# Performance work log

Measured on AMD Instinct MI355X. Metric: run time of the kernel, lower is better.

The kernel has to match this reference:

```python
import jax, jax.numpy as jnp
import numpy as np

DIM = 3072
NUM_HEADS = 24
HEAD_DIM = DIM // NUM_HEADS  # 128
SEQ = 2048
BATCH = 1


def rms_norm(x, scale):
    # compute in fp32 like the torch module
    xf = x.astype(jnp.float32)
    rrms = jax.lax.rsqrt(jnp.mean(xf * xf, axis=-1, keepdims=True) + 1e-6)
    return (xf * rrms).astype(x.dtype) * scale


def apply_rope(xq, xk, pe):
    # xq, xk: [B, H, L, D]; pe: [B, 1, L, D//2, 2, 2]
    shp = xq.shape
    xq_ = xq.reshape(*shp[:-1], -1, 1, 2).astype(jnp.float32)
    xk_ = xk.reshape(*shp[:-1], -1, 1, 2).astype(jnp.float32)
    xq_out = pe[..., 0] * xq_[..., 0] + pe[..., 1] * xq_[..., 1]
    xk_out = pe[..., 0] * xk_[..., 0] + pe[..., 1] * xk_[..., 1]
    return xq_out.reshape(shp).astype(xq.dtype), xk_out.reshape(shp).astype(xk.dtype)


def setup_inputs() -> dict:
    key = jax.random.key(0)
    ks = jax.random.split(key, 6)
    s = 1.0 / np.sqrt(DIM)
    return {
        "x": jax.random.normal(ks[0], (BATCH, SEQ, DIM), dtype=jnp.float32),
        "pe": jax.random.normal(ks[1], (BATCH, 1, SEQ, HEAD_DIM // 2, 2, 2), dtype=jnp.float32),
        "w_qkv": jax.random.normal(ks[2], (3 * DIM, DIM), dtype=jnp.float32) * s,
        "w_proj": jax.random.normal(ks[3], (DIM, DIM), dtype=jnp.float32) * s,
        "b_proj": jax.random.normal(ks[4], (DIM,), dtype=jnp.float32) * 0.01,
        "q_scale": jnp.ones((HEAD_DIM,), dtype=jnp.float32),
        "k_scale": jnp.ones((HEAD_DIM,), dtype=jnp.float32),
    }


def reference(x, pe, w_qkv, w_proj, b_proj, q_scale, k_scale):
    B, L, _ = x.shape
    # fused qkv projection (qkv_bias=False)
    qkv = jnp.einsum("bld,ed->ble", x, w_qkv)  # [B, L, 3*DIM]
    qkv = qkv.reshape(B, L, 3, NUM_HEADS, HEAD_DIM)
    qkv = jnp.transpose(qkv, (2, 0, 3, 1, 4))  # [3, B, H, L, D]
    q, k, v = qkv[0], qkv[1], qkv[2]
    # QKNorm (RMSNorm on head_dim)
    q = rms_norm(q, q_scale).astype(v.dtype)
    k = rms_norm(k, k_scale).astype(v.dtype)
    # rope
    q, k = apply_rope(q, k, pe)
    # scaled dot-product attention
    scale = 1.0 / np.sqrt(HEAD_DIM)
    scores = jnp.einsum("bhqd,bhkd->bhqk", q, k) * scale
    probs = jax.nn.softmax(scores, axis=-1)
    out = jnp.einsum("bhqk,bhkd->bhqd", probs, v)
    out = jnp.transpose(out, (0, 2, 1, 3)).reshape(B, L, DIM)  # merge heads
    # output projection
    return jnp.einsum("bld,ed->ble", out, w_proj) + b_proj
```

## Files before the change

### kernel.cpp

```cpp
#include <hip/hip_runtime.h>

typedef __bf16 bf16;
typedef __attribute__((ext_vector_type(8))) __bf16 bf16x8;
typedef __attribute__((ext_vector_type(4))) float f32x4;

typedef __attribute__((address_space(1))) void gvoid_t;
typedef __attribute__((address_space(3))) void lvoid_t;

#define LDS_LOAD16(gp, lp) \
    __builtin_amdgcn_global_load_lds((gvoid_t*)(gp), (lvoid_t*)(lp), 16, 0, 0)

__global__ __launch_bounds__(256)
void f32_to_bf16(const float* __restrict__ in, bf16* __restrict__ out, int n8)
{
    const int i = blockIdx.x * 256 + threadIdx.x;
    if (i >= n8) return;
    const float4 a = ((const float4*)in)[i * 2];
    const float4 b = ((const float4*)in)[i * 2 + 1];
    bf16x8 o;
    o[0] = (bf16)a.x; o[1] = (bf16)a.y; o[2] = (bf16)a.z; o[3] = (bf16)a.w;
    o[4] = (bf16)b.x; o[5] = (bf16)b.y; o[6] = (bf16)b.z; o[7] = (bf16)b.w;
    *(bf16x8*)(out + (size_t)i * 8) = o;
}

template <int BIAS, typename CT>
__global__ __launch_bounds__(256, 2)
void gemm_bt(const bf16* __restrict__ A, const bf16* __restrict__ B,
             const float* __restrict__ bias, CT* __restrict__ C,
             int K, int ldc)
{
    __shared__ bf16 sA[128 * 32];
    __shared__ bf16 sB[128 * 32];
    const int tid  = threadIdx.x;
    const int lane = tid & 63;
    const int wid  = tid >> 6;
    const int m0 = blockIdx.y * 128;
    const int n0 = blockIdx.x * 128;
    const int wm = (wid >> 1) * 64;
    const int wn = (wid & 1) * 64;
    const int l15   = lane & 15;
    const int quad8 = (lane >> 4) * 8;

    f32x4 acc[4][4] = {};

    for (int k0 = 0; k0 < K; k0 += 32) {
#pragma unroll
        for (int t = 0; t < 2; ++t) {
            const int e  = (t * 4 + wid) * 512;
            const int ge = e + lane * 8;
            const int r = ge >> 5, c = ge & 31;
            LDS_LOAD16(A + (size_t)(m0 + r) * K + k0 + c, sA + e);
            LDS_LOAD16(B + (size_t)(n0 + r) * K + k0 + c, sB + e);
        }
        __syncthreads();

        bf16x8 af[4], bfr[4];
#pragma unroll
        for (int i = 0; i < 4; ++i) {
            af[i]  = *(const bf16x8*)(sA + (wm + i * 16 + l15) * 32 + quad8);
            bfr[i] = *(const bf16x8*)(sB + (wn + i * 16 + l15) * 32 + quad8);
        }
#pragma unroll
        for (int i = 0; i < 4; ++i)
#pragma unroll
            for (int j = 0; j < 4; ++j)
                acc[i][j] = __builtin_amdgcn_mfma_f32_16x16x32_bf16(af[i], bfr[j], acc[i][j], 0, 0, 0);
        __syncthreads();
    }

    const int rowBase = m0 + wm + (lane >> 4) * 4;
    const int colBase = n0 + wn + l15;
#pragma unroll
    for (int j = 0; j < 4; ++j) {
        const int col = colBase + j * 16;
        const float bv = BIAS ? bias[col] : 0.0f;
#pragma unroll
        for (int i = 0; i < 4; ++i) {
            const int row = rowBase + i * 16;
#pragma unroll
            for (int r = 0; r < 4; ++r)
                C[(size_t)(row + r) * ldc + col] = (CT)(acc[i][j][r] + bv);
        }
    }
}

template <int BIAS, typename CT>
__global__ __launch_bounds__(512, 4)
void gemm128_bt(const bf16* __restrict__ A, const bf16* __restrict__ B,
                const float* __restrict__ bias, CT* __restrict__ C,
                int K, int ldc)
{
    __shared__ bf16 sA[2 * 128 * 64];
    __shared__ bf16 sB[2 * 192 * 64];

    const int tid  = threadIdx.x;
    const int lane = tid & 63;
    const int wid  = tid >> 6;
    const int m0 = blockIdx.y * 128;
    const int n0 = blockIdx.x * 192;
    const int wm = (wid >> 2) * 64;
    const int wn = (wid & 3) * 48;
    const int l15  = lane & 15;
    const int quad = lane >> 4;

    int aoff[2], boff[3];
    int adst[2], bdst[3];
#pragma unroll
    for (int t = 0; t < 2; ++t) {
        const int slot = t * 512 + tid;
        const int r  = slot >> 3;
        const int cg = (slot & 7) ^ (r & 7);
        aoff[t] = (m0 + r) * K + cg * 8;
        adst[t] = (t * 512 + wid * 64) * 8;
    }
#pragma unroll
    for (int t = 0; t < 3; ++t) {
        const int slot = t * 512 + tid;
        const int r  = slot >> 3;
        const int cg = (slot & 7) ^ (r & 7);
        boff[t] = (n0 + r) * K + cg * 8;
        bdst[t] = (t * 512 + wid * 64) * 8;
    }

#define STA(t, kt, buf) LDS_LOAD16(A + (size_t)aoff[t] + (kt) * 64, sA + (buf) * 8192  + adst[t])
#define STB(t, kt, buf) LDS_LOAD16(B + (size_t)boff[t] + (kt) * 64, sB + (buf) * 12288 + bdst[t])

    int aRd[2], bRd[2];
#pragma unroll
    for (int kk = 0; kk < 2; ++kk) {
        const int pcg = (kk * 4 + quad) ^ (l15 & 7);
        aRd[kk] = (wm + l15) * 128 + pcg * 16;
        bRd[kk] = (wn + l15) * 128 + pcg * 16;
    }

    f32x4 acc[4][3] = {};

#pragma unroll
    for (int t = 0; t < 2; ++t) STA(t, 0, 0);
#pragma unroll
    for (int t = 0; t < 3; ++t) STB(t, 0, 0);
    asm volatile("s_waitcnt vmcnt(0)" ::: "memory");

    const int NT = K >> 6;
#pragma unroll 1
    for (int u = 0; u < NT; ++u) {
        const int b = u & 1;
        __builtin_amdgcn_s_barrier();
        if (u + 1 < NT) {
            STA(0, u + 1, b ^ 1); STA(1, u + 1, b ^ 1);
            STB(0, u + 1, b ^ 1); STB(1, u + 1, b ^ 1); STB(2, u + 1, b ^ 1);
        }
        __builtin_amdgcn_sched_barrier(0);

        bf16x8 af[4][2], bfr[3][2];
#pragma unroll
        for (int mi = 0; mi < 2; ++mi)
#pragma unroll
            for (int kk = 0; kk < 2; ++kk)
                af[mi][kk] = *(const bf16x8*)((const char*)sA + b * 16384 +
                                              aRd[kk] + mi * 2048);
#pragma unroll
        for (int nf = 0; nf < 3; ++nf)
#pragma unroll
            for (int kk = 0; kk < 2; ++kk)
                bfr[nf][kk] = *(const bf16x8*)((const char*)sB + b * 24576 +
                                               bRd[kk] + nf * 2048);
        __builtin_amdgcn_sched_barrier(0);
#pragma unroll
        for (int mi = 2; mi < 4; ++mi)
#pragma unroll
            for (int kk = 0; kk < 2; ++kk)
                af[mi][kk] = *(const bf16x8*)((const char*)sA + b * 16384 +
                                              aRd[kk] + mi * 2048);
        __builtin_amdgcn_sched_barrier(0);

        asm volatile("s_waitcnt lgkmcnt(4)" ::: "memory");
        __builtin_amdgcn_sched_barrier(0);
        __builtin_amdgcn_s_setprio(1);
#pragma unroll
        for (int mi = 0; mi < 2; ++mi)
#pragma unroll
            for (int nf = 0; nf < 3; ++nf)
#pragma unroll
                for (int kk = 0; kk < 2; ++kk)
                    acc[mi][nf] = __builtin_amdgcn_mfma_f32_16x16x32_bf16(
                        af[mi][kk], bfr[nf][kk], acc[mi][nf], 0, 0, 0);
        __builtin_amdgcn_sched_barrier(0);
        asm volatile("s_waitcnt lgkmcnt(0)" ::: "memory");
        __builtin_amdgcn_sched_barrier(0);
#pragma unroll
        for (int mi = 2; mi < 4; ++mi)
#pragma unroll
            for (int nf = 0; nf < 3; ++nf)
#pragma unroll
                for (int kk = 0; kk < 2; ++kk)
                    acc[mi][nf] = __builtin_amdgcn_mfma_f32_16x16x32_bf16(
                        af[mi][kk], bfr[nf][kk], acc[mi][nf], 0, 0, 0);
        __builtin_amdgcn_s_setprio(0);
        __builtin_amdgcn_sched_barrier(0);
        asm volatile("s_waitcnt vmcnt(0)" ::: "memory");
    }
#undef STA
#undef STB

    const int rowBase = m0 + wm + quad * 4;
    const int colBase = n0 + wn + l15;
#pragma unroll
    for (int nf = 0; nf < 3; ++nf) {
        const int col = colBase + nf * 16;
        const float bv = BIAS ? bias[col] : 0.0f;
#pragma unroll
        for (int mf = 0; mf < 4; ++mf) {
            const int row = rowBase + mf * 16;
#pragma unroll
            for (int r = 0; r < 4; ++r)
                C[(size_t)(row + r) * ldc + col] = (CT)(acc[mf][nf][r] + bv);
        }
    }
}

template <int BIAS, typename CT>
__global__ __launch_bounds__(512, 4)
void gemm64_bt(const bf16* __restrict__ A, const bf16* __restrict__ B,
               const float* __restrict__ bias, CT* __restrict__ C,
               int K, int ldc)
{
    __shared__ bf16 sA[2 * 64 * 64];
    __shared__ bf16 sB[2 * 192 * 64];

    const int tid  = threadIdx.x;
    const int lane = tid & 63;
    const int wid  = tid >> 6;
    const int m0 = blockIdx.y * 64;
    const int n0 = blockIdx.x * 192;
    const int wm = (wid >> 2) * 32;
    const int wn = (wid & 3) * 48;
    const int l15  = lane & 15;
    const int quad = lane >> 4;

    int aoff, adst;
    {
        const int slot = tid;
        const int r  = slot >> 3;
        const int cg = (slot & 7) ^ (r & 7);
        aoff = (m0 + r) * K + cg * 8;
        adst = (wid * 64) * 8;
    }
    int boff[3], bdst[3];
#pragma unroll
    for (int t = 0; t < 3; ++t) {
        const int slot = t * 512 + tid;
        const int r  = slot >> 3;
        const int cg = (slot & 7) ^ (r & 7);
        boff[t] = (n0 + r) * K + cg * 8;
        bdst[t] = (t * 512 + wid * 64) * 8;
    }

#define STA64(kt, buf)    LDS_LOAD16(A + (size_t)aoff    + (kt) * 64, sA + (buf) * 4096  + adst)
#define STB64(t, kt, buf) LDS_LOAD16(B + (size_t)boff[t] + (kt) * 64, sB + (buf) * 12288 + bdst[t])

    int aRd[2], bRd[2];
#pragma unroll
    for (int kk = 0; kk < 2; ++kk) {
        const int pcg = (kk * 4 + quad) ^ (l15 & 7);
        aRd[kk] = (wm + l15) * 128 + pcg * 16;
        bRd[kk] = (wn + l15) * 128 + pcg * 16;
    }

    f32x4 acc[2][3] = {};

    STA64(0, 0);
#pragma unroll
    for (int t = 0; t < 3; ++t) STB64(t, 0, 0);
    asm volatile("s_waitcnt vmcnt(0)" ::: "memory");

    const int NT = K >> 6;
#pragma unroll 1
    for (int u = 0; u < NT; ++u) {
        const int b = u & 1;
        __builtin_amdgcn_s_barrier();
        if (u + 1 < NT) {
            STA64(u + 1, b ^ 1);
            STB64(0, u + 1, b ^ 1); STB64(1, u + 1, b ^ 1); STB64(2, u + 1, b ^ 1);
        }
        __builtin_amdgcn_sched_barrier(0);

        bf16x8 af[2][2], bfr[3][2];
#pragma unroll
        for (int kk = 0; kk < 2; ++kk)
            af[0][kk] = *(const bf16x8*)((const char*)sA + b * 8192 + aRd[kk]);
#pragma unroll
        for (int nf = 0; nf < 3; ++nf)
#pragma unroll
            for (int kk = 0; kk < 2; ++kk)
                bfr[nf][kk] = *(const bf16x8*)((const char*)sB + b * 24576 +
                                               bRd[kk] + nf * 2048);
        __builtin_amdgcn_sched_barrier(0);
#pragma unroll
        for (int kk = 0; kk < 2; ++kk)
            af[1][kk] = *(const bf16x8*)((const char*)sA + b * 8192 + aRd[kk] + 2048);
        __builtin_amdgcn_sched_barrier(0);

        asm volatile("s_waitcnt lgkmcnt(2)" ::: "memory");
        __builtin_amdgcn_sched_barrier(0);
        __builtin_amdgcn_s_setprio(1);
#pragma unroll
        for (int nf = 0; nf < 3; ++nf)
#pragma unroll
            for (int kk = 0; kk < 2; ++kk)
                acc[0][nf] = __builtin_amdgcn_mfma_f32_16x16x32_bf16(
                    af[0][kk], bfr[nf][kk], acc[0][nf], 0, 0, 0);
        __builtin_amdgcn_sched_barrier(0);
        asm volatile("s_waitcnt lgkmcnt(0)" ::: "memory");
        __builtin_amdgcn_sched_barrier(0);
#pragma unroll
        for (int nf = 0; nf < 3; ++nf)
#pragma unroll
            for (int kk = 0; kk < 2; ++kk)
                acc[1][nf] = __builtin_amdgcn_mfma_f32_16x16x32_bf16(
                    af[1][kk], bfr[nf][kk], acc[1][nf], 0, 0, 0);
        __builtin_amdgcn_s_setprio(0);
        __builtin_amdgcn_sched_barrier(0);
        asm volatile("s_waitcnt vmcnt(0)" ::: "memory");
    }
#undef STA64
#undef STB64

    const int rowBase = m0 + wm + quad * 4;
    const int colBase = n0 + wn + l15;
#pragma unroll
    for (int nf = 0; nf < 3; ++nf) {
        const int col = colBase + nf * 16;
        const float bv = BIAS ? bias[col] : 0.0f;
#pragma unroll
        for (int mf = 0; mf < 2; ++mf) {
            const int row = rowBase + mf * 16;
#pragma unroll
            for (int r = 0; r < 4; ++r)
                C[(size_t)(row + r) * ldc + col] = (CT)(acc[mf][nf][r] + bv);
        }
    }
}

__global__ __launch_bounds__(256)
void qk_rope_rearrange(const bf16* __restrict__ qkv, const float* __restrict__ pe,
                       const float* __restrict__ qs, const float* __restrict__ ks,
                       bf16* __restrict__ Qh, bf16* __restrict__ Kh, bf16* __restrict__ Vt)
{
    const int lane = threadIdx.x & 63;
    const int wid  = threadIdx.x >> 6;
    const int idx  = blockIdx.x * 4 + wid;
    const int h = idx >> 11;
    const int l = idx & 2047;

    const size_t rowb = (size_t)l * 9216 + h * 128 + 2 * lane;
    const float q0 = (float)qkv[rowb];
    const float q1 = (float)qkv[rowb + 1];
    const float k0 = (float)qkv[rowb + 3072];
    const float k1 = (float)qkv[rowb + 3073];
    const bf16  v0 = qkv[rowb + 6144];
    const bf16  v1 = qkv[rowb + 6145];

    float ssq = q0 * q0 + q1 * q1;
    float ssk = k0 * k0 + k1 * k1;
#pragma unroll
    for (int off = 1; off < 64; off <<= 1) {
        ssq += __shfl_xor(ssq, off);
        ssk += __shfl_xor(ssk, off);
    }
    const float rq = rsqrtf(ssq * (1.0f / 128.0f) + 1e-6f);
    const float rk = rsqrtf(ssk * (1.0f / 128.0f) + 1e-6f);

    const float s0q = qs[2 * lane], s1q = qs[2 * lane + 1];
    const float s0k = ks[2 * lane], s1k = ks[2 * lane + 1];

    const float qn0 = (q0 * rq) * s0q;
    const float qn1 = (q1 * rq) * s1q;
    const float kn0 = (k0 * rk) * s0k;
    const float kn1 = (k1 * rk) * s1k;

    const float* pp = pe + ((size_t)l * 64 + lane) * 4;
    const float p00 = pp[0], p01 = pp[1];
    const float p10 = pp[2], p11 = pp[3];

    const bf16 qo0 = (bf16)(p00 * qn0 + p01 * qn1);
    const bf16 qo1 = (bf16)(p10 * qn0 + p11 * qn1);
    const bf16 ko0 = (bf16)(p00 * kn0 + p01 * kn1);
    const bf16 ko1 = (bf16)(p10 * kn0 + p11 * kn1);

    const size_t ob = ((size_t)h * 2048 + l) * 128 + 2 * lane;
    Qh[ob] = qo0; Qh[ob + 1] = qo1;
    Kh[ob] = ko0; Kh[ob + 1] = ko1;

    const size_t vb = ((size_t)h * 128 + 2 * lane) * 2048 + l;
    Vt[vb]        = v0;
    Vt[vb + 2048] = v1;
}

__global__ __launch_bounds__(256, 2)
void flash_attn(const bf16* __restrict__ Qh, const bf16* __restrict__ Kh,
                const bf16* __restrict__ Vt, bf16* __restrict__ AO)
{
    __shared__ bf16 sK[2 * 64 * 128];
    __shared__ bf16 sV[2 * 128 * 64];
    __shared__ bf16 sP[4 * 16 * 72];

    const int tid   = threadIdx.x;
    const int lane  = tid & 63;
    const int wid   = tid >> 6;
    const int h     = blockIdx.y;
    const int qw    = blockIdx.x * 64 + wid * 16;
    const int l15   = lane & 15;
    const int quad  = lane >> 4;
    const int quad8 = quad * 8;

    const bf16* Kbase = Kh + (size_t)h * 2048 * 128;
    const bf16* Vbase = Vt + (size_t)h * 128 * 2048;

    bf16x8 aq[4];
    {
        const bf16* qp = Qh + ((size_t)h * 2048 + qw + l15) * 128 + quad8;
#pragma unroll
        for (int ki = 0; ki < 4; ++ki) aq[ki] = *(const bf16x8*)(qp + ki * 32);
    }

    bf16x8 ones;
#pragma unroll
    for (int i = 0; i < 8; ++i) ones[i] = (bf16)1.0f;

    f32x4 o[8] = {};
    f32x4 lacc = {};

    bf16* sPw = sP + wid * (16 * 72);
    const int slotbase = wid * 64;

#define STAGE_K(kv, buf)                                                         \
    {                                                                            \
        bf16* kb = sK + (buf) * (64 * 128);                                      \
        _Pragma("unroll")                                                        \
        for (int t = 0; t < 4; ++t) {                                            \
            const int sb   = t * 256 + slotbase;                                 \
            const int slot = sb + lane;                                          \
            const int r    = slot >> 4;                                          \
            const int cg   = (slot & 15) ^ (r & 7);                              \
            LDS_LOAD16(Kbase + (size_t)((kv) + r) * 128 + cg * 8, kb + sb * 8);  \
        }                                                                        \
    }
#define STAGE_V(kv, buf)                                                         \
    {                                                                            \
        bf16* vb = sV + (buf) * (128 * 64);                                      \
        _Pragma("unroll")                                                        \
        for (int t = 0; t < 4; ++t) {                                            \
            const int sb   = t * 256 + slotbase;                                 \
            const int slot = sb + lane;                                          \
            const int r    = slot >> 3;                                          \
            const int cg   = (slot & 7) ^ (r & 7);                               \
            LDS_LOAD16(Vbase + (size_t)r * 2048 + (kv) + cg * 8, vb + sb * 8);   \
        }                                                                        \
    }

    STAGE_K(0, 0);
    STAGE_V(0, 0);

    for (int s = 0; s < 32; ++s) {
        __syncthreads();
        if (s < 31) {
            STAGE_K((s + 1) * 64, (s + 1) & 1);
            STAGE_V((s + 1) * 64, (s + 1) & 1);
        }

        const bf16* kb = sK + (s & 1) * (64 * 128);
        const bf16* vb = sV + (s & 1) * (128 * 64);

        f32x4 sc[4];
        __builtin_amdgcn_s_setprio(1);
#pragma unroll
        for (int nt = 0; nt < 4; ++nt) {
            f32x4 t = {};
            const int row = nt * 16 + l15;
#pragma unroll
            for (int ki = 0; ki < 4; ++ki) {
                const int pcg = (4 * ki + quad) ^ (l15 & 7);
                bf16x8 bk = *(const bf16x8*)(kb + row * 128 + pcg * 8);
                t = __builtin_amdgcn_mfma_f32_16x16x32_bf16(aq[ki], bk, t, 0, 0, 0);
            }
            sc[nt] = t;
        }
        __builtin_amdgcn_s_setprio(0);

#pragma unroll
        for (int r = 0; r < 4; ++r) {
            const float scl = 0.08838834764831845f;
            bf16* pw = sPw + (quad * 4 + r) * 72 + l15;
            pw[0]  = (bf16)__expf(sc[0][r] * scl);
            pw[16] = (bf16)__expf(sc[1][r] * scl);
            pw[32] = (bf16)__expf(sc[2][r] * scl);
            pw[48] = (bf16)__expf(sc[3][r] * scl);
        }

        __builtin_amdgcn_s_setprio(1);
#pragma unroll
        for (int kk = 0; kk < 2; ++kk) {
            bf16x8 pa = *(const bf16x8*)(sPw + l15 * 72 + kk * 32 + quad8);
            lacc = __builtin_amdgcn_mfma_f32_16x16x32_bf16(pa, ones, lacc, 0, 0, 0);
#pragma unroll
            for (int dt = 0; dt < 8; ++dt) {
                const int row = dt * 16 + l15;
                const int pcg = (kk * 4 + quad) ^ (l15 & 7);
                bf16x8 bv = *(const bf16x8*)(vb + row * 64 + pcg * 8);
                o[dt] = __builtin_amdgcn_mfma_f32_16x16x32_bf16(pa, bv, o[dt], 0, 0, 0);
            }
        }
        __builtin_amdgcn_s_setprio(0);
    }
#undef STAGE_K
#undef STAGE_V

#pragma unroll
    for (int r = 0; r < 4; ++r) {
        const float inv = 1.0f / lacc[r];
        const size_t row = qw + quad * 4 + r;
        bf16* op = AO + row * 3072 + h * 128 + l15;
#pragma unroll
        for (int dt = 0; dt < 8; ++dt) op[dt * 16] = (bf16)(o[dt][r] * inv);
    }
}

extern "C" void kernel_launch(void* const* d_in, const int* in_sizes, int n_in,
                              void* d_out, int out_size, void* d_ws, size_t ws_size,
                              hipStream_t stream)
{
    (void)in_sizes; (void)n_in; (void)out_size;

    const float* x      = (const float*)d_in[0];
    const float* pe     = (const float*)d_in[1];
    const float* w_qkv  = (const float*)d_in[2];
    const float* w_proj = (const float*)d_in[3];
    const float* b_proj = (const float*)d_in[4];
    const float* q_s    = (const float*)d_in[5];
    const float* k_s    = (const float*)d_in[6];
    float* out = (float*)d_out;

    const size_t NEED_BIG = ((size_t)6291456 + 28311552 + 18874368 + 6291456) * 2;

    if (ws_size >= NEED_BIG) {
        bf16* xb  = (bf16*)d_ws;
        bf16* wb  = xb + (size_t)6291456;
        bf16* qkv = wb + (size_t)28311552;
        bf16* Vt  = qkv + (size_t)18874368;
        bf16* Qh  = xb;
        bf16* Kh  = wb;
        bf16* wpb = qkv;
        bf16* AO  = qkv + (size_t)9437184;

        f32_to_bf16<<<dim3(3072),  256, 0, stream>>>(x,     xb, 786432);
        f32_to_bf16<<<dim3(13824), 256, 0, stream>>>(w_qkv, wb, 3538944);
        gemm128_bt<0, bf16><<<dim3(48, 16), 512, 0, stream>>>(xb, wb, nullptr, qkv, 3072, 9216);
        qk_rope_rearrange<<<dim3(12288), 256, 0, stream>>>(qkv, pe, q_s, k_s, Qh, Kh, Vt);
        f32_to_bf16<<<dim3(4608), 256, 0, stream>>>(w_proj, wpb, 1179648);
        flash_attn<<<dim3(32, 24), 256, 0, stream>>>(Qh, Kh, Vt, AO);
        gemm64_bt<1, float><<<dim3(16, 32), 512, 0, stream>>>(AO, wpb, b_proj, out, 3072, 3072);
    } else {
        bf16* xb  = (bf16*)d_ws;
        bf16* wb  = xb + (size_t)6291456;
        bf16* qkv = wb + (size_t)9437184;
        bf16* Vt  = qkv + (size_t)18874368;
        bf16* Qh  = xb;
        bf16* Kh  = wb;
        bf16* wpb = qkv;
        bf16* AO  = qkv + (size_t)9437184;

        f32_to_bf16<<<dim3(3072), 256, 0, stream>>>(x, xb, 786432);
        for (int c = 0; c < 3; ++c) {
            f32_to_bf16<<<dim3(4608), 256, 0, stream>>>(w_qkv + (size_t)c * 9437184, wb, 1179648);
            gemm_bt<0, bf16><<<dim3(24, 16), 256, 0, stream>>>(xb, wb, nullptr, qkv + c * 3072, 3072, 9216);
        }
        qk_rope_rearrange<<<dim3(12288), 256, 0, stream>>>(qkv, pe, q_s, k_s, Qh, Kh, Vt);
        f32_to_bf16<<<dim3(4608), 256, 0, stream>>>(w_proj, wpb, 1179648);
        flash_attn<<<dim3(32, 24), 256, 0, stream>>>(Qh, Kh, Vt, AO);
        gemm64_bt<1, float><<<dim3(16, 32), 512, 0, stream>>>(AO, wpb, b_proj, out, 3072, 3072);
    }
}
```

Measured before the change: 535.3 us.

## Halve GEMM block threads and give each wave a larger output tile

Both the QKV and output-projection GEMM kernels go from 8 waves to 4 waves per block while keeping the same block tile. Each wave now computes twice the output (64x96 or 64x48), loading more fragments per k-step and reusing them across more MFMAs. This cuts LDS read traffic per MFMA and barrier participants, but raises register pressure with 24 accumulators per wave and leaves fewer waves per block to hide latency.

```diff
diff --git a/kernel.cpp b/kernel.cpp
--- a/kernel.cpp
+++ b/kernel.cpp
@@ -85,7 +85,7 @@
 }
 
 template <int BIAS, typename CT>
-__global__ __launch_bounds__(512, 4)
+__global__ __launch_bounds__(256, 2)
 void gemm128_bt(const bf16* __restrict__ A, const bf16* __restrict__ B,
                 const float* __restrict__ bias, CT* __restrict__ C,
                 int K, int ldc)
@@ -98,28 +98,28 @@
     const int wid  = tid >> 6;
     const int m0 = blockIdx.y * 128;
     const int n0 = blockIdx.x * 192;
-    const int wm = (wid >> 2) * 64;
-    const int wn = (wid & 3) * 48;
+    const int wm = (wid >> 1) * 64;
+    const int wn = (wid & 1) * 96;
     const int l15  = lane & 15;
     const int quad = lane >> 4;
 
-    int aoff[2], boff[3];
-    int adst[2], bdst[3];
-#pragma unroll
-    for (int t = 0; t < 2; ++t) {
-        const int slot = t * 512 + tid;
+    int aoff[4], boff[6];
+    int adst[4], bdst[6];
+#pragma unroll
+    for (int t = 0; t < 4; ++t) {
+        const int slot = t * 256 + tid;
         const int r  = slot >> 3;
         const int cg = (slot & 7) ^ (r & 7);
         aoff[t] = (m0 + r) * K + cg * 8;
-        adst[t] = (t * 512 + wid * 64) * 8;
-    }
-#pragma unroll
-    for (int t = 0; t < 3; ++t) {
-        const int slot = t * 512 + tid;
+        adst[t] = (t * 256 + wid * 64) * 8;
+    }
+#pragma unroll
+    for (int t = 0; t < 6; ++t) {
+        const int slot = t * 256 + tid;
         const int r  = slot >> 3;
         const int cg = (slot & 7) ^ (r & 7);
         boff[t] = (n0 + r) * K + cg * 8;
-        bdst[t] = (t * 512 + wid * 64) * 8;
+        bdst[t] = (t * 256 + wid * 64) * 8;
     }
 
 #define STA(t, kt, buf) LDS_LOAD16(A + (size_t)aoff[t] + (kt) * 64, sA + (buf) * 8192  + adst[t])
@@ -133,12 +133,12 @@
         bRd[kk] = (wn + l15) * 128 + pcg * 16;
     }
 
-    f32x4 acc[4][3] = {};
-
-#pragma unroll
-    for (int t = 0; t < 2; ++t) STA(t, 0, 0);
-#pragma unroll
-    for (int t = 0; t < 3; ++t) STB(t, 0, 0);
+    f32x4 acc[4][6] = {};
+
+#pragma unroll
+    for (int t = 0; t < 4; ++t) STA(t, 0, 0);
+#pragma unroll
+    for (int t = 0; t < 6; ++t) STB(t, 0, 0);
     asm volatile("s_waitcnt vmcnt(0)" ::: "memory");
 
     const int NT = K >> 6;
@@ -148,13 +148,15 @@
         __builtin_amdgcn_s_barrier();
         if (u + 1 < NT) {
             STA(0, u + 1, b ^ 1); STA(1, u + 1, b ^ 1);
+            STA(2, u + 1, b ^ 1); STA(3, u + 1, b ^ 1);
             STB(0, u + 1, b ^ 1); STB(1, u + 1, b ^ 1); STB(2, u + 1, b ^ 1);
-        }
-        __builtin_amdgcn_sched_barrier(0);
-
-        bf16x8 af[4][2], bfr[3][2];
-#pragma unroll
-        for (int mi = 0; mi < 2; ++mi)
+            STB(3, u + 1, b ^ 1); STB(4, u + 1, b ^ 1); STB(5, u + 1, b ^ 1);
+        }
+        __builtin_amdgcn_sched_barrier(0);
+
+        bf16x8 af[4][2], bfr[6][2];
+#pragma unroll
+        for (int mi = 0; mi < 4; ++mi)
 #pragma unroll
             for (int kk = 0; kk < 2; ++kk)
                 af[mi][kk] = *(const bf16x8*)((const char*)sA + b * 16384 +
@@ -167,18 +169,18 @@
                                                bRd[kk] + nf * 2048);
         __builtin_amdgcn_sched_barrier(0);
 #pragma unroll
-        for (int mi = 2; mi < 4; ++mi)
+        for (int nf = 3; nf < 6; ++nf)
 #pragma unroll
             for (int kk = 0; kk < 2; ++kk)
-                af[mi][kk] = *(const bf16x8*)((const char*)sA + b * 16384 +
-                                              aRd[kk] + mi * 2048);
-        __builtin_amdgcn_sched_barrier(0);
-
-        asm volatile("s_waitcnt lgkmcnt(4)" ::: "memory");
+                bfr[nf][kk] = *(const bf16x8*)((const char*)sB + b * 24576 +
+                                               bRd[kk] + nf * 2048);
+        __builtin_amdgcn_sched_barrier(0);
+
+        asm volatile("s_waitcnt lgkmcnt(6)" ::: "memory");
         __builtin_amdgcn_sched_barrier(0);
         __builtin_amdgcn_s_setprio(1);
 #pragma unroll
-        for (int mi = 0; mi < 2; ++mi)
+        for (int mi = 0; mi < 4; ++mi)
 #pragma unroll
             for (int nf = 0; nf < 3; ++nf)
 #pragma unroll
@@ -189,9 +191,9 @@
         asm volatile("s_waitcnt lgkmcnt(0)" ::: "memory");
         __builtin_amdgcn_sched_barrier(0);
 #pragma unroll
-        for (int mi = 2; mi < 4; ++mi)
-#pragma unroll
-            for (int nf = 0; nf < 3; ++nf)
+        for (int mi = 0; mi < 4; ++mi)
+#pragma unroll
+            for (int nf = 3; nf < 6; ++nf)
 #pragma unroll
                 for (int kk = 0; kk < 2; ++kk)
                     acc[mi][nf] = __builtin_amdgcn_mfma_f32_16x16x32_bf16(
@@ -206,7 +208,7 @@
     const int rowBase = m0 + wm + quad * 4;
     const int colBase = n0 + wn + l15;
 #pragma unroll
-    for (int nf = 0; nf < 3; ++nf) {
+    for (int nf = 0; nf < 6; ++nf) {
         const int col = colBase + nf * 16;
         const float bv = BIAS ? bias[col] : 0.0f;
 #pragma unroll
@@ -220,7 +222,7 @@
 }
 
 template <int BIAS, typename CT>
-__global__ __launch_bounds__(512, 4)
+__global__ __launch_bounds__(256, 2)
 void gemm64_bt(const bf16* __restrict__ A, const bf16* __restrict__ B,
                const float* __restrict__ bias, CT* __restrict__ C,
                int K, int ldc)
@@ -233,45 +235,45 @@
     const int wid  = tid >> 6;
     const int m0 = blockIdx.y * 64;
     const int n0 = blockIdx.x * 192;
-    const int wm = (wid >> 2) * 32;
-    const int wn = (wid & 3) * 48;
+    const int wn = wid * 48;
     const int l15  = lane & 15;
     const int quad = lane >> 4;
 
-    int aoff, adst;
-    {
-        const int slot = tid;
+    int aoff[2], adst[2], boff[6], bdst[6];
+#pragma unroll
+    for (int t = 0; t < 2; ++t) {
+        const int slot = t * 256 + tid;
         const int r  = slot >> 3;
         const int cg = (slot & 7) ^ (r & 7);
-        aoff = (m0 + r) * K + cg * 8;
-        adst = (wid * 64) * 8;
-    }
-    int boff[3], bdst[3];
-#pragma unroll
-    for (int t = 0; t < 3; ++t) {
-        const int slot = t * 512 + tid;
+        aoff[t] = (m0 + r) * K + cg * 8;
+        adst[t] = (t * 256 + wid * 64) * 8;
+    }
+#pragma unroll
+    for (int t = 0; t < 6; ++t) {
+        const int slot = t * 256 + tid;
         const int r  = slot >> 3;
         const int cg = (slot & 7) ^ (r & 7);
         boff[t] = (n0 + r) * K + cg * 8;
-        bdst[t] = (t * 512 + wid * 64) * 8;
-    }
-
-#define STA64(kt, buf)    LDS_LOAD16(A + (size_t)aoff    + (kt) * 64, sA + (buf) * 4096  + adst)
+        bdst[t] = (t * 256 + wid * 64) * 8;
+    }
+
+#define STA64(t, kt, buf) LDS_LOAD16(A + (size_t)aoff[t] + (kt) * 64, sA + (buf) * 4096  + adst[t])
 #define STB64(t, kt, buf) LDS_LOAD16(B + (size_t)boff[t] + (kt) * 64, sB + (buf) * 12288 + bdst[t])
 
     int aRd[2], bRd[2];
 #pragma unroll
     for (int kk = 0; kk < 2; ++kk) {
         const int pcg = (kk * 4 + quad) ^ (l15 & 7);
-        aRd[kk] = (wm + l15) * 128 + pcg * 16;
+        aRd[kk] = l15 * 128 + pcg * 16;
         bRd[kk] = (wn + l15) * 128 + pcg * 16;
     }
 
-    f32x4 acc[2][3] = {};
-
-    STA64(0, 0);
-#pragma unroll
-    for (int t = 0; t < 3; ++t) STB64(t, 0, 0);
+    f32x4 acc[4][3] = {};
+
+#pragma unroll
+    for (int t = 0; t < 2; ++t) STA64(t, 0, 0);
+#pragma unroll
+    for (int t = 0; t < 6; ++t) STB64(t, 0, 0);
     asm volatile("s_waitcnt vmcnt(0)" ::: "memory");
 
     const int NT = K >> 6;
@@ -280,17 +282,21 @@
         const int b = u & 1;
         __builtin_amdgcn_s_barrier();
         if (u + 1 < NT) {
-            STA64(u + 1, b ^ 1);
+            STA64(0, u + 1, b ^ 1); STA64(1, u + 1, b ^ 1);
             STB64(0, u + 1, b ^ 1); STB64(1, u + 1, b ^ 1); STB64(2, u + 1, b ^ 1);
-        }
-        __builtin_amdgcn_sched_barrier(0);
-
-        bf16x8 af[2][2], bfr[3][2];
-#pragma unroll
-        for (int kk = 0; kk < 2; ++kk)
-            af[0][kk] = *(const bf16x8*)((const char*)sA + b * 8192 + aRd[kk]);
-#pragma unroll
-        for (int nf = 0; nf < 3; ++nf)
+            STB64(3, u + 1, b ^ 1); STB64(4, u + 1, b ^ 1); STB64(5, u + 1, b ^ 1);
+        }
+        __builtin_amdgcn_sched_barrier(0);
+
+        bf16x8 af[4][2], bfr[3][2];
+#pragma unroll
+        for (int mi = 0; mi < 4; ++mi)
+#pragma unroll
+            for (int kk = 0; kk < 2; ++kk)
+                af[mi][kk] = *(const bf16x8*)((const char*)sA + b * 8192 +
+                                              aRd[kk] + mi * 2048);
+#pragma unroll
+        for (int nf = 0; nf < 2; ++nf)
 #pragma unroll
             for (int kk = 0; kk < 2; ++kk)
                 bfr[nf][kk] = *(const bf16x8*)((const char*)sB + b * 24576 +
@@ -298,27 +304,30 @@
         __builtin_amdgcn_sched_barrier(0);
 #pragma unroll
         for (int kk = 0; kk < 2; ++kk)
-            af[1][kk] = *(const bf16x8*)((const char*)sA + b * 8192 + aRd[kk] + 2048);
+            bfr[2][kk] = *(const bf16x8*)((const char*)sB + b * 24576 +
+                                          bRd[kk] + 2 * 2048);
         __builtin_amdgcn_sched_barrier(0);
 
         asm volatile("s_waitcnt lgkmcnt(2)" ::: "memory");
         __builtin_amdgcn_sched_barrier(0);
         __builtin_amdgcn_s_setprio(1);
 #pragma unroll
-        for (int nf = 0; nf < 3; ++nf)
+        for (int mi = 0; mi < 4; ++mi)
+#pragma unroll
+            for (int nf = 0; nf < 2; ++nf)
+#pragma unroll
+                for (int kk = 0; kk < 2; ++kk)
+                    acc[mi][nf] = __builtin_amdgcn_mfma_f32_16x16x32_bf16(
+                        af[mi][kk], bfr[nf][kk], acc[mi][nf], 0, 0, 0);
+        __builtin_amdgcn_sched_barrier(0);
+        asm volatile("s_waitcnt lgkmcnt(0)" ::: "memory");
+        __builtin_amdgcn_sched_barrier(0);
+#pragma unroll
+        for (int mi = 0; mi < 4; ++mi)
 #pragma unroll
             for (int kk = 0; kk < 2; ++kk)
-                acc[0][nf] = __builtin_amdgcn_mfma_f32_16x16x32_bf16(
-                    af[0][kk], bfr[nf][kk], acc[0][nf], 0, 0, 0);
-        __builtin_amdgcn_sched_barrier(0);
-        asm volatile("s_waitcnt lgkmcnt(0)" ::: "memory");
-        __builtin_amdgcn_sched_barrier(0);
-#pragma unroll
-        for (int nf = 0; nf < 3; ++nf)
-#pragma unroll
-            for (int kk = 0; kk < 2; ++kk)
-                acc[1][nf] = __builtin_amdgcn_mfma_f32_16x16x32_bf16(
-                    af[1][kk], bfr[nf][kk], acc[1][nf], 0, 0, 0);
+                acc[mi][2] = __builtin_amdgcn_mfma_f32_16x16x32_bf16(
+                    af[mi][kk], bfr[2][kk], acc[mi][2], 0, 0, 0);
         __builtin_amdgcn_s_setprio(0);
         __builtin_amdgcn_sched_barrier(0);
         asm volatile("s_waitcnt vmcnt(0)" ::: "memory");
@@ -326,14 +335,14 @@
 #undef STA64
 #undef STB64
 
-    const int rowBase = m0 + wm + quad * 4;
+    const int rowBase = m0 + quad * 4;
     const int colBase = n0 + wn + l15;
 #pragma unroll
     for (int nf = 0; nf < 3; ++nf) {
         const int col = colBase + nf * 16;
         const float bv = BIAS ? bias[col] : 0.0f;
 #pragma unroll
-        for (int mf = 0; mf < 2; ++mf) {
+        for (int mf = 0; mf < 4; ++mf) {
             const int row = rowBase + mf * 16;
 #pragma unroll
             for (int r = 0; r < 4; ++r)
@@ -555,11 +564,11 @@
 
         f32_to_bf16<<<dim3(3072),  256, 0, stream>>>(x,     xb, 786432);
         f32_to_bf16<<<dim3(13824), 256, 0, stream>>>(w_qkv, wb, 3538944);
-        gemm128_bt<0, bf16><<<dim3(48, 16), 512, 0, stream>>>(xb, wb, nullptr, qkv, 3072, 9216);
+        gemm128_bt<0, bf16><<<dim3(48, 16), 256, 0, stream>>>(xb, wb, nullptr, qkv, 3072, 9216);
         qk_rope_rearrange<<<dim3(12288), 256, 0, stream>>>(qkv, pe, q_s, k_s, Qh, Kh, Vt);
         f32_to_bf16<<<dim3(4608), 256, 0, stream>>>(w_proj, wpb, 1179648);
         flash_attn<<<dim3(32, 24), 256, 0, stream>>>(Qh, Kh, Vt, AO);
-        gemm64_bt<1, float><<<dim3(16, 32), 512, 0, stream>>>(AO, wpb, b_proj, out, 3072, 3072);
+        gemm64_bt<1, float><<<dim3(16, 32), 256, 0, stream>>>(AO, wpb, b_proj, out, 3072, 3072);
     } else {
         bf16* xb  = (bf16*)d_ws;
         bf16* wb  = xb + (size_t)6291456;
@@ -578,6 +587,6 @@
         qk_rope_rearrange<<<dim3(12288), 256, 0, stream>>>(qkv, pe, q_s, k_s, Qh, Kh, Vt);
         f32_to_bf16<<<dim3(4608), 256, 0, stream>>>(w_proj, wpb, 1179648);
         flash_attn<<<dim3(32, 24), 256, 0, stream>>>(Qh, Kh, Vt, AO);
-        gemm64_bt<1, float><<<dim3(16, 32), 512, 0, stream>>>(AO, wpb, b_proj, out, 3072, 3072);
-    }
-}
+        gemm64_bt<1, float><<<dim3(16, 32), 256, 0, stream>>>(AO, wpb, b_proj, out, 3072, 3072);
+    }
+}
```

Measured after the change: 540.0 us. About the same (+0.9%).
